# Kernel tuning notes

Hardware: AMD Instinct MI355X
Metric: run time of the kernel (lower is better)

Reference implementation:

```python
import jax, jax.numpy as jnp
import numpy as np

B, S, D, H, DFF = 2, 2048, 2048, 16, 8192
DH = D // H
EPS = 1e-5


def _layer_norm(x, g, b):
    mu = jnp.mean(x, axis=-1, keepdims=True)
    var = jnp.mean(jnp.square(x - mu), axis=-1, keepdims=True)
    return (x - mu) * jax.lax.rsqrt(var + EPS) * g + b


def setup_inputs() -> dict:
    key = jax.random.key(0)
    ks = jax.random.split(key, 12)
    sc = 0.02
    inp = {
        "x": jax.random.normal(ks[0], (B, S, D), dtype=jnp.float32),
        # attention projections, stored [in, out] (torch Linear weight transposed)
        "wq": jax.random.normal(ks[1], (D, D), dtype=jnp.float32) * sc,
        "bq": jnp.zeros((D,), jnp.float32),
        "wk": jax.random.normal(ks[2], (D, D), dtype=jnp.float32) * sc,
        "bk": jnp.zeros((D,), jnp.float32),
        "wv": jax.random.normal(ks[3], (D, D), dtype=jnp.float32) * sc,
        "bv": jnp.zeros((D,), jnp.float32),
        "wo": jax.random.normal(ks[4], (D, D), dtype=jnp.float32) * sc,
        "bo": jnp.zeros((D,), jnp.float32),
        "ln1_g": jnp.ones((D,), jnp.float32),
        "ln1_b": jnp.zeros((D,), jnp.float32),
        # feed-forward
        "w1": jax.random.normal(ks[5], (D, DFF), dtype=jnp.float32) * sc,
        "b1": jnp.zeros((DFF,), jnp.float32),
        "w2": jax.random.normal(ks[6], (DFF, D), dtype=jnp.float32) * sc,
        "b2": jnp.zeros((D,), jnp.float32),
        "ln2_g": jnp.ones((D,), jnp.float32),
        "ln2_b": jnp.zeros((D,), jnp.float32),
    }
    return inp


def reference(x, wq, bq, wk, bk, wv, bv, wo, bo, ln1_g, ln1_b,
              w1, b1, w2, b2, ln2_g, ln2_b):
    # ---- MultiHeadAttentionBlock: x + MHA(LN(x)) ----
    h = _layer_norm(x, ln1_g, ln1_b)                      # [B,S,D]
    q = (h @ wq + bq).reshape(B, S, H, DH).transpose(0, 2, 1, 3)  # [B,H,S,DH]
    k = (h @ wk + bk).reshape(B, S, H, DH).transpose(0, 2, 1, 3)
    v = (h @ wv + bv).reshape(B, S, H, DH).transpose(0, 2, 1, 3)

    # faithful to source: scale by sqrt(d_dim), NOT sqrt(head_dim)
    scores = jnp.einsum("bhqd,bhkd->bhqk", q, k) / np.sqrt(D).astype(np.float32)
    # faithful triu/transpose masking (softmax sees raw zeros, not -inf)
    t = jnp.triu(scores).swapaxes(-2, -1)                 # [B,H,S,S]
    s = jax.nn.softmax(t, axis=-2)
    r = jnp.triu(s).swapaxes(-2, -1)
    attn = jnp.einsum("bhqk,bhkd->bhqd", r, v)            # [B,H,S,DH]
    attn = attn.transpose(0, 2, 1, 3).reshape(B, S, D)
    x = x + attn @ wo + bo

    # ---- FeedForwardBlock: x + FF(LN(x)), dropout rate 0 ----
    h2 = _layer_norm(x, ln2_g, ln2_b)
    ff = jax.nn.relu(h2 @ w1 + b1) @ w2 + b2
    return x + ff
```

## Files before the change

kernel.cpp:

```cpp
#include <hip/hip_runtime.h>


typedef unsigned short ushort_t;
typedef unsigned int   uint32;
typedef __attribute__((ext_vector_type(8)))  short    short8;
typedef __attribute__((ext_vector_type(8)))  ushort_t ushort8;
typedef __attribute__((ext_vector_type(4)))  float    f32x4;

#define BDIM   2
#define SEQ    2048
#define DMODEL 2048
#define NHEAD  16
#define DHEAD  128
#define DFFN   8192
#define MROWS  (BDIM*SEQ)
#define LDQKV  6144

#define GPTR(p) (const __attribute__((address_space(1))) void*)((const void*)(p))
#define SPTR(p) (__attribute__((address_space(3))) void*)((void*)(p))

__device__ __forceinline__ float bf2f(ushort_t u) {
  union { uint32 i; float f; } c; c.i = ((uint32)u) << 16; return c.f;
}
__device__ __forceinline__ ushort_t f2bf(float f) {
  union { float f; uint32 i; } c; c.f = f;
  uint32 u = c.i;
  return (ushort_t)((u + 0x7fffu + ((u >> 16) & 1u)) >> 16);
}

__global__ __launch_bounds__(256) void prep_kern(
    const float* __restrict__ wq, const float* __restrict__ wk,
    const float* __restrict__ wv, const float* __restrict__ wo,
    const float* __restrict__ w1, const float* __restrict__ w2,
    const float* __restrict__ bq, const float* __restrict__ bk,
    const float* __restrict__ bv,
    ushort_t* __restrict__ WQKV, ushort_t* __restrict__ WOT,
    ushort_t* __restrict__ W1T, ushort_t* __restrict__ W2T,
    float* __restrict__ Bcat)
{
  const int bid = blockIdx.x;
  if (bid >= 49152) {
    for (int i = threadIdx.x; i < 6144; i += 256)
      Bcat[i] = (i < 2048) ? bq[i] : ((i < 4096) ? bk[i - 2048] : bv[i - 4096]);
    return;
  }
  const float* W; ushort_t* Wt; int K, N, local;
  if (bid < 12288) {
    const int which = bid >> 12; local = bid & 4095;
    W = (which == 0) ? wq : (which == 1) ? wk : wv;
    Wt = WQKV + (size_t)which * 2048 * 2048; K = 2048; N = 2048;
  } else if (bid < 16384) { W = wo; Wt = WOT; K = 2048; N = 2048; local = bid - 12288; }
  else if (bid < 32768)   { W = w1; Wt = W1T; K = 2048; N = 8192; local = bid - 16384; }
  else                    { W = w2; Wt = W2T; K = 8192; N = 2048; local = bid - 32768; }
  const int ntiles = N >> 5;
  const int nb = (local % ntiles) * 32, kb = (local / ntiles) * 32;

  __shared__ float tile[32][33];
  const int tx = threadIdx.x & 31, ty = threadIdx.x >> 5;
#pragma unroll
  for (int j = 0; j < 32; j += 8)
    tile[ty + j][tx] = W[(size_t)(kb + ty + j) * N + nb + tx];
  __syncthreads();
#pragma unroll
  for (int j = 0; j < 32; j += 8)
    Wt[(size_t)(nb + ty + j) * K + kb + tx] = f2bf(tile[tx][ty + j]);
}

__global__ __launch_bounds__(256) void ln_kern(
    const float* __restrict__ X, const float* __restrict__ G,
    const float* __restrict__ Bb, ushort_t* __restrict__ Out)
{
  const int row = blockIdx.x, tid = threadIdx.x;
  const float* xr = X + (size_t)row * DMODEL;
  float4 v0 = ((const float4*)xr)[tid * 2];
  float4 v1 = ((const float4*)xr)[tid * 2 + 1];
  float s  = v0.x + v0.y + v0.z + v0.w + v1.x + v1.y + v1.z + v1.w;
  float ss = v0.x*v0.x + v0.y*v0.y + v0.z*v0.z + v0.w*v0.w
           + v1.x*v1.x + v1.y*v1.y + v1.z*v1.z + v1.w*v1.w;
#pragma unroll
  for (int off = 32; off > 0; off >>= 1) {
    s  += __shfl_down(s, off);
    ss += __shfl_down(ss, off);
  }
  __shared__ float rs[4], rss[4];
  __shared__ float sh_mu, sh_rst;
  const int wv = tid >> 6;
  if ((tid & 63) == 0) { rs[wv] = s; rss[wv] = ss; }
  __syncthreads();
  if (tid == 0) {
    float S1 = rs[0] + rs[1] + rs[2] + rs[3];
    float S2 = rss[0] + rss[1] + rss[2] + rss[3];
    float mu = S1 * (1.f / DMODEL);
    float var = S2 * (1.f / DMODEL) - mu * mu;
    sh_mu = mu;
    sh_rst = rsqrtf(var + 1e-5f);
  }
  __syncthreads();
  const float mu = sh_mu, rst = sh_rst;
  float4 g0 = ((const float4*)G)[tid * 2];
  float4 g1 = ((const float4*)G)[tid * 2 + 1];
  float4 b0 = ((const float4*)Bb)[tid * 2];
  float4 b1 = ((const float4*)Bb)[tid * 2 + 1];
  ushort8 o;
  o[0] = f2bf((v0.x - mu) * rst * g0.x + b0.x);
  o[1] = f2bf((v0.y - mu) * rst * g0.y + b0.y);
  o[2] = f2bf((v0.z - mu) * rst * g0.z + b0.z);
  o[3] = f2bf((v0.w - mu) * rst * g0.w + b0.w);
  o[4] = f2bf((v1.x - mu) * rst * g1.x + b1.x);
  o[5] = f2bf((v1.y - mu) * rst * g1.y + b1.y);
  o[6] = f2bf((v1.z - mu) * rst * g1.z + b1.z);
  o[7] = f2bf((v1.w - mu) * rst * g1.w + b1.w);
  *(ushort8*)(Out + (size_t)row * DMODEL + tid * 8) = o;
}

__global__ __launch_bounds__(256) void combine_ln_kern(
    const ushort_t* __restrict__ pp, const float* __restrict__ bias,
    const float* __restrict__ xres, const float* __restrict__ G,
    const float* __restrict__ Bb, float* __restrict__ X2,
    ushort_t* __restrict__ Out)
{
  const int row = blockIdx.x, tid = threadIdx.x;
  const size_t i = (size_t)row * DMODEL + tid * 8;
  ushort8 p0 = *(const ushort8*)(pp + i);
  ushort8 p1 = *(const ushort8*)(pp + (size_t)MROWS * 2048 + i);
  float v[8];
#pragma unroll
  for (int j = 0; j < 8; ++j)
    v[j] = bf2f(p0[j]) + bf2f(p1[j]) + bias[tid * 8 + j] + xres[i + j];
  float4 o0 = {v[0], v[1], v[2], v[3]}, o1 = {v[4], v[5], v[6], v[7]};
  *(float4*)(X2 + i) = o0;
  *(float4*)(X2 + i + 4) = o1;

  float s = 0.f, ss = 0.f;
#pragma unroll
  for (int j = 0; j < 8; ++j) { s += v[j]; ss += v[j] * v[j]; }
#pragma unroll
  for (int off = 32; off > 0; off >>= 1) {
    s  += __shfl_down(s, off);
    ss += __shfl_down(ss, off);
  }
  __shared__ float rs[4], rss[4];
  __shared__ float sh_mu, sh_rst;
  const int wvv = tid >> 6;
  if ((tid & 63) == 0) { rs[wvv] = s; rss[wvv] = ss; }
  __syncthreads();
  if (tid == 0) {
    float S1 = rs[0] + rs[1] + rs[2] + rs[3];
    float S2 = rss[0] + rss[1] + rss[2] + rss[3];
    float mu = S1 * (1.f / DMODEL);
    float var = S2 * (1.f / DMODEL) - mu * mu;
    sh_mu = mu; sh_rst = rsqrtf(var + 1e-5f);
  }
  __syncthreads();
  const float mu = sh_mu, rst = sh_rst;
  ushort8 o;
#pragma unroll
  for (int j = 0; j < 8; ++j)
    o[j] = f2bf((v[j] - mu) * rst * G[tid * 8 + j] + Bb[tid * 8 + j]);
  *(ushort8*)(Out + i) = o;
}

template<int OUT, int RELU, int KDIV>
__global__ __launch_bounds__(512, 2) void gemm8_kern(
    const ushort_t* __restrict__ A, const ushort_t* __restrict__ Bt,
    const float* __restrict__ bias, void* __restrict__ Cout,
    int M, int N, int K)
{
  __shared__ ushort_t sA[4 * 8192];
  __shared__ ushort_t sB[4 * 8192];

  const int tid = threadIdx.x;
  const int nM  = gridDim.y;
  const int nwg = gridDim.x * nM;
  const int bid = blockIdx.y * gridDim.x + blockIdx.x;
  const int cpx = nwg >> 3;
  const int swz = (bid & 7) * cpx + (bid >> 3);
  const int m0 = (swz % nM) * 256;
  const int n0 = (swz / nM) * 256;

  const int Keff = K / KDIV;
  const int k0 = (KDIV > 1) ? blockIdx.z * Keff : 0;
  const int T = Keff >> 6;

  const int l = tid & 63, w = tid >> 6;
  const int lr = l & 15, lg = l >> 4;
  const int wr = w >> 2, wc = w & 3;

  const int xch   = (lg ^ ((lr >> 1) & 3)) * 8;
  const int abase = (wr * 128 + lr) * 32 + xch;
  const int bbase = (wc * 64  + lr) * 32 + xch;

  const int sr = tid >> 2;
  const int sg = ((tid & 3) ^ ((tid >> 3) & 3)) * 8;
  const ushort_t* Asrc = A  + (size_t)(m0 + sr) * K + k0 + sg;
  const ushort_t* Bsrc = Bt + (size_t)(n0 + sr) * K + k0 + sg;
  ushort_t* dA = sA + tid * 8;
  ushort_t* dB = sB + tid * 8;

#define SA_(slot, kt, kk, r) __builtin_amdgcn_global_load_lds( \
    GPTR(Asrc + (size_t)(r) * 128 * K + (kt) * 64 + (kk) * 32), \
    SPTR(dA + (slot) * 8192 + (r) * 4096), 16, 0, 0)
#define SB_(slot, kt, kk, r) __builtin_amdgcn_global_load_lds( \
    GPTR(Bsrc + (size_t)(r) * 128 * K + (kt) * 64 + (kk) * 32), \
    SPTR(dB + (slot) * 8192 + (r) * 4096), 16, 0, 0)

  f32x4 acc[8][4] = {};

  SA_(0, 0, 0, 0); SA_(0, 0, 0, 1); SB_(0, 0, 0, 0); SB_(0, 0, 0, 1);
  SA_(1, 0, 1, 0); SA_(1, 0, 1, 1); SB_(1, 0, 1, 0); SB_(1, 0, 1, 1);
  SA_(2, 1, 0, 0); SA_(2, 1, 0, 1); SB_(2, 1, 0, 0); SB_(2, 1, 0, 1);
  asm volatile("s_waitcnt vmcnt(8)" ::: "memory");
  __builtin_amdgcn_s_barrier();

  for (int t = 0; t < T; ++t) {
    const int c = t & 1;
    const ushort_t* A0 = sA + (c * 2 + 0) * 8192;
    const ushort_t* B0 = sB + (c * 2 + 0) * 8192;
    const ushort_t* A1 = sA + (c * 2 + 1) * 8192;
    const ushort_t* B1 = sB + (c * 2 + 1) * 8192;
    const int s1 = (c ^ 1) * 2 + 1;
    const int s0 = c * 2;
    const bool pf1 = (t + 1 < T), pf0 = (t + 2 < T);
    const bool last2 = (t >= T - 2);

    short8 a0, a1, a2, a3, b0, b1, b2, b3;

    b0 = *(const short8*)(B0 + bbase);
    b1 = *(const short8*)(B0 + bbase + 512);
    b2 = *(const short8*)(B0 + bbase + 1024);
    b3 = *(const short8*)(B0 + bbase + 1536);
    a0 = *(const short8*)(A0 + abase);
    a1 = *(const short8*)(A0 + abase + 512);
    a2 = *(const short8*)(A0 + abase + 1024);
    a3 = *(const short8*)(A0 + abase + 1536);
    if (pf1) { SA_(s1, t + 1, 1, 0); SA_(s1, t + 1, 1, 1); }
    __builtin_amdgcn_s_setprio(1);
    acc[0][0] = __builtin_amdgcn_mfma_f32_16x16x32_bf16(a0, b0, acc[0][0], 0, 0, 0);
    acc[0][1] = __builtin_amdgcn_mfma_f32_16x16x32_bf16(a0, b1, acc[0][1], 0, 0, 0);
    acc[0][2] = __builtin_amdgcn_mfma_f32_16x16x32_bf16(a0, b2, acc[0][2], 0, 0, 0);
    acc[0][3] = __builtin_amdgcn_mfma_f32_16x16x32_bf16(a0, b3, acc[0][3], 0, 0, 0);
    acc[1][0] = __builtin_amdgcn_mfma_f32_16x16x32_bf16(a1, b0, acc[1][0], 0, 0, 0);
    acc[1][1] = __builtin_amdgcn_mfma_f32_16x16x32_bf16(a1, b1, acc[1][1], 0, 0, 0);
    acc[1][2] = __builtin_amdgcn_mfma_f32_16x16x32_bf16(a1, b2, acc[1][2], 0, 0, 0);
    acc[1][3] = __builtin_amdgcn_mfma_f32_16x16x32_bf16(a1, b3, acc[1][3], 0, 0, 0);
    acc[2][0] = __builtin_amdgcn_mfma_f32_16x16x32_bf16(a2, b0, acc[2][0], 0, 0, 0);
    acc[2][1] = __builtin_amdgcn_mfma_f32_16x16x32_bf16(a2, b1, acc[2][1], 0, 0, 0);
    acc[2][2] = __builtin_amdgcn_mfma_f32_16x16x32_bf16(a2, b2, acc[2][2], 0, 0, 0);
    acc[2][3] = __builtin_amdgcn_mfma_f32_16x16x32_bf16(a2, b3, acc[2][3], 0, 0, 0);
    acc[3][0] = __builtin_amdgcn_mfma_f32_16x16x32_bf16(a3, b0, acc[3][0], 0, 0, 0);
    acc[3][1] = __builtin_amdgcn_mfma_f32_16x16x32_bf16(a3, b1, acc[3][1], 0, 0, 0);
    acc[3][2] = __builtin_amdgcn_mfma_f32_16x16x32_bf16(a3, b2, acc[3][2], 0, 0, 0);
    acc[3][3] = __builtin_amdgcn_mfma_f32_16x16x32_bf16(a3, b3, acc[3][3], 0, 0, 0);
    __builtin_amdgcn_s_setprio(0);

    a0 = *(const short8*)(A0 + abase + 2048);
    a1 = *(const short8*)(A0 + abase + 2560);
    a2 = *(const short8*)(A0 + abase + 3072);
    a3 = *(const short8*)(A0 + abase + 3584);
    if (pf1) { SB_(s1, t + 1, 1, 0); SB_(s1, t + 1, 1, 1); }
    __builtin_amdgcn_s_setprio(1);
    acc[4][0] = __builtin_amdgcn_mfma_f32_16x16x32_bf16(a0, b0, acc[4][0], 0, 0, 0);
    acc[4][1] = __builtin_amdgcn_mfma_f32_16x16x32_bf16(a0, b1, acc[4][1], 0, 0, 0);
    acc[4][2] = __builtin_amdgcn_mfma_f32_16x16x32_bf16(a0, b2, acc[4][2], 0, 0, 0);
    acc[4][3] = __builtin_amdgcn_mfma_f32_16x16x32_bf16(a0, b3, acc[4][3], 0, 0, 0);
    acc[5][0] = __builtin_amdgcn_mfma_f32_16x16x32_bf16(a1, b0, acc[5][0], 0, 0, 0);
    acc[5][1] = __builtin_amdgcn_mfma_f32_16x16x32_bf16(a1, b1, acc[5][1], 0, 0, 0);
    acc[5][2] = __builtin_amdgcn_mfma_f32_16x16x32_bf16(a1, b2, acc[5][2], 0, 0, 0);
    acc[5][3] = __builtin_amdgcn_mfma_f32_16x16x32_bf16(a1, b3, acc[5][3], 0, 0, 0);
    acc[6][0] = __builtin_amdgcn_mfma_f32_16x16x32_bf16(a2, b0, acc[6][0], 0, 0, 0);
    acc[6][1] = __builtin_amdgcn_mfma_f32_16x16x32_bf16(a2, b1, acc[6][1], 0, 0, 0);
    acc[6][2] = __builtin_amdgcn_mfma_f32_16x16x32_bf16(a2, b2, acc[6][2], 0, 0, 0);
    acc[6][3] = __builtin_amdgcn_mfma_f32_16x16x32_bf16(a2, b3, acc[6][3], 0, 0, 0);
    acc[7][0] = __builtin_amdgcn_mfma_f32_16x16x32_bf16(a3, b0, acc[7][0], 0, 0, 0);
    acc[7][1] = __builtin_amdgcn_mfma_f32_16x16x32_bf16(a3, b1, acc[7][1], 0, 0, 0);
    acc[7][2] = __builtin_amdgcn_mfma_f32_16x16x32_bf16(a3, b2, acc[7][2], 0, 0, 0);
    acc[7][3] = __builtin_amdgcn_mfma_f32_16x16x32_bf16(a3, b3, acc[7][3], 0, 0, 0);
    __builtin_amdgcn_s_setprio(0);
    if (!last2) { asm volatile("s_waitcnt vmcnt(8)" ::: "memory"); }
    else        { asm volatile("s_waitcnt vmcnt(0)" ::: "memory"); }
    __builtin_amdgcn_s_barrier();

    b0 = *(const short8*)(B1 + bbase);
    b1 = *(const short8*)(B1 + bbase + 512);
    b2 = *(const short8*)(B1 + bbase + 1024);
    b3 = *(const short8*)(B1 + bbase + 1536);
    a0 = *(const short8*)(A1 + abase);
    a1 = *(const short8*)(A1 + abase + 512);
    a2 = *(const short8*)(A1 + abase + 1024);
    a3 = *(const short8*)(A1 + abase + 1536);
    if (pf0) { SA_(s0, t + 2, 0, 0); SA_(s0, t + 2, 0, 1); }
    __builtin_amdgcn_s_setprio(1);
    acc[0][0] = __builtin_amdgcn_mfma_f32_16x16x32_bf16(a0, b0, acc[0][0], 0, 0, 0);
    acc[0][1] = __builtin_amdgcn_mfma_f32_16x16x32_bf16(a0, b1, acc[0][1], 0, 0, 0);
    acc[0][2] = __builtin_amdgcn_mfma_f32_16x16x32_bf16(a0, b2, acc[0][2], 0, 0, 0);
    acc[0][3] = __builtin_amdgcn_mfma_f32_16x16x32_bf16(a0, b3, acc[0][3], 0, 0, 0);
    acc[1][0] = __builtin_amdgcn_mfma_f32_16x16x32_bf16(a1, b0, acc[1][0], 0, 0, 0);
    acc[1][1] = __builtin_amdgcn_mfma_f32_16x16x32_bf16(a1, b1, acc[1][1], 0, 0, 0);
    acc[1][2] = __builtin_amdgcn_mfma_f32_16x16x32_bf16(a1, b2, acc[1][2], 0, 0, 0);
    acc[1][3] = __builtin_amdgcn_mfma_f32_16x16x32_bf16(a1, b3, acc[1][3], 0, 0, 0);
    acc[2][0] = __builtin_amdgcn_mfma_f32_16x16x32_bf16(a2, b0, acc[2][0], 0, 0, 0);
    acc[2][1] = __builtin_amdgcn_mfma_f32_16x16x32_bf16(a2, b1, acc[2][1], 0, 0, 0);
    acc[2][2] = __builtin_amdgcn_mfma_f32_16x16x32_bf16(a2, b2, acc[2][2], 0, 0, 0);
    acc[2][3] = __builtin_amdgcn_mfma_f32_16x16x32_bf16(a2, b3, acc[2][3], 0, 0, 0);
    acc[3][0] = __builtin_amdgcn_mfma_f32_16x16x32_bf16(a3, b0, acc[3][0], 0, 0, 0);
    acc[3][1] = __builtin_amdgcn_mfma_f32_16x16x32_bf16(a3, b1, acc[3][1], 0, 0, 0);
    acc[3][2] = __builtin_amdgcn_mfma_f32_16x16x32_bf16(a3, b2, acc[3][2], 0, 0, 0);
    acc[3][3] = __builtin_amdgcn_mfma_f32_16x16x32_bf16(a3, b3, acc[3][3], 0, 0, 0);
    __builtin_amdgcn_s_setprio(0);

    a0 = *(const short8*)(A1 + abase + 2048);
    a1 = *(const short8*)(A1 + abase + 2560);
    a2 = *(const short8*)(A1 + abase + 3072);
    a3 = *(const short8*)(A1 + abase + 3584);
    if (pf0) { SB_(s0, t + 2, 0, 0); SB_(s0, t + 2, 0, 1); }
    __builtin_amdgcn_s_setprio(1);
    acc[4][0] = __builtin_amdgcn_mfma_f32_16x16x32_bf16(a0, b0, acc[4][0], 0, 0, 0);
    acc[4][1] = __builtin_amdgcn_mfma_f32_16x16x32_bf16(a0, b1, acc[4][1], 0, 0, 0);
    acc[4][2] = __builtin_amdgcn_mfma_f32_16x16x32_bf16(a0, b2, acc[4][2], 0, 0, 0);
    acc[4][3] = __builtin_amdgcn_mfma_f32_16x16x32_bf16(a0, b3, acc[4][3], 0, 0, 0);
    acc[5][0] = __builtin_amdgcn_mfma_f32_16x16x32_bf16(a1, b0, acc[5][0], 0, 0, 0);
    acc[5][1] = __builtin_amdgcn_mfma_f32_16x16x32_bf16(a1, b1, acc[5][1], 0, 0, 0);
    acc[5][2] = __builtin_amdgcn_mfma_f32_16x16x32_bf16(a1, b2, acc[5][2], 0, 0, 0);
    acc[5][3] = __builtin_amdgcn_mfma_f32_16x16x32_bf16(a1, b3, acc[5][3], 0, 0, 0);
    acc[6][0] = __builtin_amdgcn_mfma_f32_16x16x32_bf16(a2, b0, acc[6][0], 0, 0, 0);
    acc[6][1] = __builtin_amdgcn_mfma_f32_16x16x32_bf16(a2, b1, acc[6][1], 0, 0, 0);
    acc[6][2] = __builtin_amdgcn_mfma_f32_16x16x32_bf16(a2, b2, acc[6][2], 0, 0, 0);
    acc[6][3] = __builtin_amdgcn_mfma_f32_16x16x32_bf16(a2, b3, acc[6][3], 0, 0, 0);
    acc[7][0] = __builtin_amdgcn_mfma_f32_16x16x32_bf16(a3, b0, acc[7][0], 0, 0, 0);
    acc[7][1] = __builtin_amdgcn_mfma_f32_16x16x32_bf16(a3, b1, acc[7][1], 0, 0, 0);
    acc[7][2] = __builtin_amdgcn_mfma_f32_16x16x32_bf16(a3, b2, acc[7][2], 0, 0, 0);
    acc[7][3] = __builtin_amdgcn_mfma_f32_16x16x32_bf16(a3, b3, acc[7][3], 0, 0, 0);
    __builtin_amdgcn_s_setprio(0);
    if (!last2) { asm volatile("s_waitcnt vmcnt(8)" ::: "memory"); }
    else        { asm volatile("s_waitcnt vmcnt(0)" ::: "memory"); }
    __builtin_amdgcn_s_barrier();
  }
#undef SA_
#undef SB_

  ushort_t* Pz = (OUT == 2)
      ? (ushort_t*)Cout + (size_t)blockIdx.z * M * N : (ushort_t*)Cout;
#pragma unroll
  for (int mi = 0; mi < 8; ++mi) {
#pragma unroll
    for (int ni = 0; ni < 4; ++ni) {
      const int gn = n0 + wc * 64 + ni * 16 + lr;
      const float bvv = (OUT == 2) ? 0.f : bias[gn];
#pragma unroll
      for (int j = 0; j < 4; ++j) {
        const int gm = m0 + wr * 128 + mi * 16 + lg * 4 + j;
        float v = acc[mi][ni][j] + bvv;
        if (RELU) v = fmaxf(v, 0.f);
        Pz[(size_t)gm * N + gn] = f2bf(v);
      }
    }
  }
}

template<int RELU>
__global__ __launch_bounds__(512) void gemm_hi_kern(
    const ushort_t* __restrict__ A, const ushort_t* __restrict__ Bt,
    const float* __restrict__ bias, ushort_t* __restrict__ Cout,
    int M, int N, int K)
{
  __shared__ ushort_t sA[3 * 4096];
  __shared__ ushort_t sB[3 * 8192];

  const int tid = threadIdx.x;
  const int nM  = gridDim.y;
  const int nwg = gridDim.x * nM;
  const int bid = blockIdx.y * gridDim.x + blockIdx.x;
  const int cpx = nwg >> 3;
  const int swz = (bid & 7) * cpx + (bid >> 3);
  const int m0 = (swz % nM) * 128;
  const int n0 = (swz / nM) * 256;

  const int l = tid & 63, w = tid >> 6;
  const int lr = l & 15, lg = l >> 4;
  const int wr = w >> 2, wc = w & 3;

  const int xch   = (lg ^ ((lr >> 1) & 3)) * 8;
  const int abase = (wr * 64 + lr) * 32 + xch;
  const int bbase = (wc * 64 + lr) * 32 + xch;

  const int sr = tid >> 2;
  const int sg = ((tid & 3) ^ ((tid >> 3) & 3)) * 8;
  const ushort_t* Asrc = A  + (size_t)(m0 + sr) * K + sg;
  const ushort_t* Bsrc = Bt + (size_t)(n0 + sr) * K + sg;
  ushort_t* dA = sA + tid * 8;
  ushort_t* dB = sB + tid * 8;

  const int U = K >> 5;

#define SAU(slot, u) __builtin_amdgcn_global_load_lds( \
    GPTR(Asrc + (size_t)(u) * 32), SPTR(dA + (slot) * 4096), 16, 0, 0)
#define SBU(slot, u, r) __builtin_amdgcn_global_load_lds( \
    GPTR(Bsrc + (size_t)(r) * 128 * K + (size_t)(u) * 32), \
    SPTR(dB + (slot) * 8192 + (r) * 4096), 16, 0, 0)

  f32x4 acc[4][4] = {};

  SAU(0, 0); SBU(0, 0, 0); SBU(0, 0, 1);
  SAU(1, 1); SBU(1, 1, 0); SBU(1, 1, 1);
  asm volatile("s_waitcnt vmcnt(3)" ::: "memory");
  __builtin_amdgcn_s_barrier();

  int cur = 0;
  for (int u = 0; u < U; ++u) {
    const ushort_t* pA = sA + cur * 4096;
    const ushort_t* pB = sB + cur * 8192;
    const int nx = (cur == 0) ? 2 : cur - 1;
    short8 af[4], bf[4];
#pragma unroll
    for (int i = 0; i < 4; ++i) af[i] = *(const short8*)(pA + abase + i * 512);
#pragma unroll
    for (int i = 0; i < 4; ++i) bf[i] = *(const short8*)(pB + bbase + i * 512);
    if (u + 2 < U) { SAU(nx, u + 2); SBU(nx, u + 2, 0); SBU(nx, u + 2, 1); }
    __builtin_amdgcn_s_setprio(1);
#pragma unroll
    for (int mi = 0; mi < 4; ++mi)
#pragma unroll
      for (int ni = 0; ni < 4; ++ni)
        acc[mi][ni] = __builtin_amdgcn_mfma_f32_16x16x32_bf16(
            af[mi], bf[ni], acc[mi][ni], 0, 0, 0);
    __builtin_amdgcn_s_setprio(0);
    if (u < U - 2) { asm volatile("s_waitcnt vmcnt(3)" ::: "memory"); }
    else           { asm volatile("s_waitcnt vmcnt(0)" ::: "memory"); }
    __builtin_amdgcn_s_barrier();
    cur = (cur == 2) ? 0 : cur + 1;
  }
#undef SAU
#undef SBU

#pragma unroll
  for (int mi = 0; mi < 4; ++mi) {
#pragma unroll
    for (int ni = 0; ni < 4; ++ni) {
      const int gn = n0 + wc * 64 + ni * 16 + lr;
      const float bvv = bias[gn];
#pragma unroll
      for (int j = 0; j < 4; ++j) {
        const int gm = m0 + wr * 64 + mi * 16 + lg * 4 + j;
        float v = acc[mi][ni][j] + bvv;
        if (RELU) v = fmaxf(v, 0.f);
        Cout[(size_t)gm * N + gn] = f2bf(v);
      }
    }
  }
}

__global__ __launch_bounds__(256) void combine_kern(
    const ushort_t* __restrict__ pp, const float* __restrict__ bias,
    const float* __restrict__ resid, float* __restrict__ out)
{
  const size_t i = ((size_t)blockIdx.x * 256 + threadIdx.x) * 8;
  ushort8 p0 = *(const ushort8*)(pp + i);
  ushort8 p1 = *(const ushort8*)(pp + (size_t)MROWS * 2048 + i);
  const int col = (int)(i & 2047);
  float4 r0 = *(const float4*)(resid + i);
  float4 r1 = *(const float4*)(resid + i + 4);
  float4 c0 = *(const float4*)(bias + col);
  float4 c1 = *(const float4*)(bias + col + 4);
  float4 o0, o1;
  o0.x = bf2f(p0[0]) + bf2f(p1[0]) + c0.x + r0.x;
  o0.y = bf2f(p0[1]) + bf2f(p1[1]) + c0.y + r0.y;
  o0.z = bf2f(p0[2]) + bf2f(p1[2]) + c0.z + r0.z;
  o0.w = bf2f(p0[3]) + bf2f(p1[3]) + c0.w + r0.w;
  o1.x = bf2f(p0[4]) + bf2f(p1[4]) + c1.x + r1.x;
  o1.y = bf2f(p0[5]) + bf2f(p1[5]) + c1.y + r1.y;
  o1.z = bf2f(p0[6]) + bf2f(p1[6]) + c1.z + r1.z;
  o1.w = bf2f(p0[7]) + bf2f(p1[7]) + c1.w + r1.w;
  *(float4*)(out + i) = o0;
  *(float4*)(out + i + 4) = o1;
}

__global__ __launch_bounds__(256) void attn_stats_kern(
    const ushort_t* __restrict__ Q, const ushort_t* __restrict__ Kb,
    float* __restrict__ E, float* __restrict__ DG, int ld)
{
  __shared__ ushort_t Ksm[64 * 128];
  const int qb = blockIdx.x;
  const int bh = blockIdx.y;
  const int b = bh >> 4, h = bh & 15;
  const int tid = threadIdx.x;
  const int l = tid & 63, w = tid >> 6;
  const int lr = l & 15, lg = l >> 4;

  const int qrow0 = qb * 128 + w * 32;

  short8 af[2][4];
#pragma unroll
  for (int g = 0; g < 2; ++g) {
    const size_t qoff = (size_t)(b * SEQ + qrow0 + g * 16 + lr) * ld + h * DHEAD + lg * 8;
#pragma unroll
    for (int c = 0; c < 4; ++c) af[g][c] = *(const short8*)(Q + qoff + c * 32);
  }

  const int srow_b = w * 16 + (l >> 4);
  const ushort_t* Kg = Kb + (size_t)b * SEQ * ld + (size_t)h * DHEAD;
  ushort_t* Sbase = Ksm + w * 2048;

  f32x4 sume[2] = {{0.f,0.f,0.f,0.f},{0.f,0.f,0.f,0.f}};
  f32x4 dge[2]  = {{0.f,0.f,0.f,0.f},{0.f,0.f,0.f,0.f}};
  const float scale = 0.0220970869120796f;
  const int rx = lr & 7;

  for (int kc = qb * 2; kc < 32; ++kc) {
    __syncthreads();
#pragma unroll
    for (int c = 0; c < 4; ++c) {
      const int row = srow_b + c * 4;
      const int g = (l & 15) ^ (row & 7);
      __builtin_amdgcn_global_load_lds(
          GPTR(Kg + (size_t)(kc * 64 + row) * ld + g * 8),
          SPTR(Sbase + c * 512), 16, 0, 0);
    }
    __syncthreads();

    for (int ks = 0; ks < 4; ++ks) {
      const int kbase = kc * 64 + ks * 16;
      if (kbase + 16 <= qrow0) continue;
      short8 bfr[4];
#pragma unroll
      for (int c = 0; c < 4; ++c)
        bfr[c] = *(const short8*)(Ksm + (ks * 16 + lr) * 128 + ((lg + c * 4) ^ rx) * 8);
#pragma unroll
      for (int g = 0; g < 2; ++g) {
        const int qg = qrow0 + g * 16;
        if (kbase < qg) continue;
        f32x4 sc = {0.f, 0.f, 0.f, 0.f};
        sc = __builtin_amdgcn_mfma_f32_16x16x32_bf16(af[g][0], bfr[0], sc, 0, 0, 0);
        sc = __builtin_amdgcn_mfma_f32_16x16x32_bf16(af[g][1], bfr[1], sc, 0, 0, 0);
        sc = __builtin_amdgcn_mfma_f32_16x16x32_bf16(af[g][2], bfr[2], sc, 0, 0, 0);
        sc = __builtin_amdgcn_mfma_f32_16x16x32_bf16(af[g][3], bfr[3], sc, 0, 0, 0);
        if (kbase == qg) {
          const int ki = kbase + lr;
#pragma unroll
          for (int j = 0; j < 4; ++j) {
            const int qi = qg + lg * 4 + j;
            if (ki >= qi) {
              float e = __expf(sc[j] * scale);
              sume[g][j] += e;
              if (ki == qi) dge[g][j] += e;
            }
          }
        } else {
#pragma unroll
          for (int j = 0; j < 4; ++j)
            sume[g][j] += __expf(sc[j] * scale);
        }
      }
    }
  }

#pragma unroll
  for (int g = 0; g < 2; ++g) {
#pragma unroll
    for (int j = 0; j < 4; ++j) {
#pragma unroll
      for (int off = 1; off < 16; off <<= 1) {
        sume[g][j] += __shfl_xor(sume[g][j], off);
        dge[g][j]  += __shfl_xor(dge[g][j], off);
      }
    }
  }
  if (lr == 0) {
#pragma unroll
    for (int g = 0; g < 2; ++g)
#pragma unroll
      for (int j = 0; j < 4; ++j) {
        E[(size_t)bh * SEQ + qrow0 + g * 16 + lg * 4 + j]  = sume[g][j];
        DG[(size_t)bh * SEQ + qrow0 + g * 16 + lg * 4 + j] = dge[g][j];
      }
  }
}

__global__ __launch_bounds__(128) void vchunk_kern(
    const ushort_t* __restrict__ V, float* __restrict__ CS, int ld)
{
  const int c = blockIdx.x, bh = blockIdx.y;
  const int b = bh >> 4, h = bh & 15;
  const int dh = threadIdx.x;
  const ushort_t* vp = V + (size_t)(b * SEQ + c * 64) * ld + h * DHEAD + dh;
  float s = 0.f;
  for (int i = 0; i < 64; ++i) s += bf2f(vp[(size_t)i * ld]);
  CS[((size_t)bh * 32 + c) * 128 + dh] = s;
}

__global__ __launch_bounds__(128) void attn_combine_kern(
    const ushort_t* __restrict__ V, const float* __restrict__ CS,
    const float* __restrict__ E, const float* __restrict__ DG,
    ushort_t* __restrict__ Attn, int ldv)
{
  const int c = blockIdx.x, bh = blockIdx.y;
  const int b = bh >> 4, h = bh & 15;
  const int dh = threadIdx.x;
  float prefix = 0.f;
  for (int cc = 0; cc < c; ++cc) prefix += CS[((size_t)bh * 32 + cc) * 128 + dh];
  const ushort_t* vp = V + (size_t)(b * SEQ + c * 64) * ldv + h * DHEAD + dh;
  ushort_t* ap = Attn + (size_t)(b * SEQ + c * 64) * DMODEL + h * DHEAD + dh;
  const int qb = c * 64;
  for (int i = 0; i < 64; ++i) {
    const int qq = qb + i;
    const float denom = (float)qq + E[(size_t)bh * SEQ + qq];
    const float de = DG[(size_t)bh * SEQ + qq];
    const float vv = bf2f(vp[(size_t)i * ldv]);
    ap[(size_t)i * DMODEL] = f2bf((prefix + de * vv) / denom);
    prefix += vv;
  }
}

extern "C" void kernel_launch(void* const* d_in, const int* in_sizes, int n_in,
                              void* d_out, int out_size, void* d_ws, size_t ws_size,
                              hipStream_t stream)
{
  const float* x    = (const float*)d_in[0];
  const float* wq   = (const float*)d_in[1];
  const float* bq   = (const float*)d_in[2];
  const float* wk   = (const float*)d_in[3];
  const float* bk   = (const float*)d_in[4];
  const float* wv   = (const float*)d_in[5];
  const float* bv   = (const float*)d_in[6];
  const float* wo   = (const float*)d_in[7];
  const float* bo   = (const float*)d_in[8];
  const float* ln1g = (const float*)d_in[9];
  const float* ln1b = (const float*)d_in[10];
  const float* w1   = (const float*)d_in[11];
  const float* b1   = (const float*)d_in[12];
  const float* w2   = (const float*)d_in[13];
  const float* b2   = (const float*)d_in[14];
  const float* ln2g = (const float*)d_in[15];
  const float* ln2b = (const float*)d_in[16];
  float* out = (float*)d_out;

  char* ws = (char*)d_ws;
  ushort_t* W1T  = (ushort_t*)(ws + 0);
  ushort_t* PPf2 = (ushort_t*)(ws + 0);
  ushort_t* W2T  = (ushort_t*)(ws + 33554432);
  ushort_t* WOT  = (ushort_t*)(ws + 67108864);
  float*    X2   = (float*)   (ws + 75497472);
  float*    Bcat = (float*)   (ws + 75497472);
  ushort_t* Hb   = (ushort_t*)(ws + 109051904);
  ushort_t* F1   = (ushort_t*)(ws + 125829120);
  ushort_t* PPwo = (ushort_t*)(ws + 125829120);
  ushort_t* WQKV = (ushort_t*)(ws + 125829120);
  ushort_t* QKVb = (ushort_t*)(ws + 150994944);
  float*    Eb   = (float*)   (ws + 201326592);
  float*    DGb  = (float*)   (ws + 201588736);
  float*    CSb  = (float*)   (ws + 201850880);

  prep_kern<<<49153, 256, 0, stream>>>(wq, wk, wv, wo, w1, w2, bq, bk, bv,
                                       WQKV, WOT, W1T, W2T, Bcat);

  ln_kern<<<MROWS, 256, 0, stream>>>(x, ln1g, ln1b, Hb);

  gemm8_kern<1, 0, 1><<<dim3(24, 16), 512, 0, stream>>>(
      Hb, WQKV, Bcat, QKVb, MROWS, LDQKV, DMODEL);

  attn_stats_kern<<<dim3(16, 32), 256, 0, stream>>>(QKVb, QKVb + 2048, Eb, DGb, LDQKV);

  vchunk_kern<<<dim3(32, 32), 128, 0, stream>>>(QKVb + 4096, CSb, LDQKV);
  attn_combine_kern<<<dim3(32, 32), 128, 0, stream>>>(QKVb + 4096, CSb, Eb, DGb, Hb, LDQKV);

  gemm8_kern<2, 0, 2><<<dim3(8, 16, 2), 512, 0, stream>>>(
      Hb, WOT, bo, PPwo, MROWS, DMODEL, DMODEL);

  combine_ln_kern<<<MROWS, 256, 0, stream>>>(PPwo, bo, x, ln2g, ln2b, X2, Hb);

  gemm_hi_kern<1><<<dim3(32, 32), 512, 0, stream>>>(
      Hb, W1T, b1, F1, MROWS, DFFN, DMODEL);

  gemm8_kern<2, 0, 2><<<dim3(8, 16, 2), 512, 0, stream>>>(
      F1, W2T, b2, PPf2, MROWS, DMODEL, DFFN);
  combine_kern<<<4096, 256, 0, stream>>>(PPf2, b2, X2, out);
}
```

Measured before the change: 631.4 us.

## Swap GEMM tile configs per layer and double-buffer K tiles in attention stats

The QKV and output-projection GEMMs now use the 128x256 three-stage kernel, which gains split-K support. The FFN1 GEMM moves to the 256x256 kernel. The attention stats kernel now double-buffers K tiles in shared memory, so the next chunk's load overlaps the current chunk's MFMA work. A residual/fp32-output path is added to gemm8 but is not used. These changes rebalance grid sizes and occupancy per GEMM shape and hide load latency in the attention pass, at the cost of more shared memory in attn_stats.

```diff
diff --git a/kernel.cpp b/kernel.cpp
--- a/kernel.cpp
+++ b/kernel.cpp
@@ -160,11 +160,11 @@
   *(ushort8*)(Out + i) = o;
 }
 
-template<int OUT, int RELU, int KDIV>
+template<int OUT, int RELU, int RESID, int KDIV>
 __global__ __launch_bounds__(512, 2) void gemm8_kern(
     const ushort_t* __restrict__ A, const ushort_t* __restrict__ Bt,
-    const float* __restrict__ bias, void* __restrict__ Cout,
-    int M, int N, int K)
+    const float* __restrict__ bias, const float* __restrict__ resid,
+    void* __restrict__ Cout, int M, int N, int K)
 {
   __shared__ ushort_t sA[4 * 8192];
   __shared__ ushort_t sB[4 * 8192];
@@ -350,14 +350,16 @@
       for (int j = 0; j < 4; ++j) {
         const int gm = m0 + wr * 128 + mi * 16 + lg * 4 + j;
         float v = acc[mi][ni][j] + bvv;
+        if (RESID) v += resid[(size_t)gm * N + gn];
         if (RELU) v = fmaxf(v, 0.f);
-        Pz[(size_t)gm * N + gn] = f2bf(v);
+        if (OUT == 0)      ((float*)Cout)[(size_t)gm * N + gn] = v;
+        else               Pz[(size_t)gm * N + gn] = f2bf(v);
       }
     }
   }
 }
 
-template<int RELU>
+template<int OUT, int RELU, int KDIV>
 __global__ __launch_bounds__(512) void gemm_hi_kern(
     const ushort_t* __restrict__ A, const ushort_t* __restrict__ Bt,
     const float* __restrict__ bias, ushort_t* __restrict__ Cout,
@@ -375,6 +377,10 @@
   const int m0 = (swz % nM) * 128;
   const int n0 = (swz / nM) * 256;
 
+  const int Keff = K / KDIV;
+  const int k0 = (KDIV > 1) ? blockIdx.z * Keff : 0;
+  const int U = Keff >> 5;
+
   const int l = tid & 63, w = tid >> 6;
   const int lr = l & 15, lg = l >> 4;
   const int wr = w >> 2, wc = w & 3;
@@ -385,12 +391,10 @@
 
   const int sr = tid >> 2;
   const int sg = ((tid & 3) ^ ((tid >> 3) & 3)) * 8;
-  const ushort_t* Asrc = A  + (size_t)(m0 + sr) * K + sg;
-  const ushort_t* Bsrc = Bt + (size_t)(n0 + sr) * K + sg;
+  const ushort_t* Asrc = A  + (size_t)(m0 + sr) * K + k0 + sg;
+  const ushort_t* Bsrc = Bt + (size_t)(n0 + sr) * K + k0 + sg;
   ushort_t* dA = sA + tid * 8;
   ushort_t* dB = sB + tid * 8;
-
-  const int U = K >> 5;
 
 #define SAU(slot, u) __builtin_amdgcn_global_load_lds( \
     GPTR(Asrc + (size_t)(u) * 32), SPTR(dA + (slot) * 4096), 16, 0, 0)
@@ -432,18 +436,20 @@
 #undef SAU
 #undef SBU
 
+  ushort_t* Pz = (OUT == 2)
+      ? Cout + (size_t)blockIdx.z * M * N : Cout;
 #pragma unroll
   for (int mi = 0; mi < 4; ++mi) {
 #pragma unroll
     for (int ni = 0; ni < 4; ++ni) {
       const int gn = n0 + wc * 64 + ni * 16 + lr;
-      const float bvv = bias[gn];
+      const float bvv = (OUT == 2) ? 0.f : bias[gn];
 #pragma unroll
       for (int j = 0; j < 4; ++j) {
         const int gm = m0 + wr * 64 + mi * 16 + lg * 4 + j;
         float v = acc[mi][ni][j] + bvv;
         if (RELU) v = fmaxf(v, 0.f);
-        Cout[(size_t)gm * N + gn] = f2bf(v);
+        Pz[(size_t)gm * N + gn] = f2bf(v);
       }
     }
   }
@@ -478,7 +484,7 @@
     const ushort_t* __restrict__ Q, const ushort_t* __restrict__ Kb,
     float* __restrict__ E, float* __restrict__ DG, int ld)
 {
-  __shared__ ushort_t Ksm[64 * 128];
+  __shared__ ushort_t Ksm[2 * 8192];
   const int qb = blockIdx.x;
   const int bh = blockIdx.y;
   const int b = bh >> 4, h = bh & 15;
@@ -498,24 +504,30 @@
 
   const int srow_b = w * 16 + (l >> 4);
   const ushort_t* Kg = Kb + (size_t)b * SEQ * ld + (size_t)h * DHEAD;
-  ushort_t* Sbase = Ksm + w * 2048;
 
   f32x4 sume[2] = {{0.f,0.f,0.f,0.f},{0.f,0.f,0.f,0.f}};
   f32x4 dge[2]  = {{0.f,0.f,0.f,0.f},{0.f,0.f,0.f,0.f}};
   const float scale = 0.0220970869120796f;
   const int rx = lr & 7;
-
-  for (int kc = qb * 2; kc < 32; ++kc) {
-    __syncthreads();
-#pragma unroll
-    for (int c = 0; c < 4; ++c) {
-      const int row = srow_b + c * 4;
-      const int g = (l & 15) ^ (row & 7);
-      __builtin_amdgcn_global_load_lds(
-          GPTR(Kg + (size_t)(kc * 64 + row) * ld + g * 8),
-          SPTR(Sbase + c * 512), 16, 0, 0);
-    }
-    __syncthreads();
+  const int kc0 = qb * 2;
+
+#define STAGEK(kc, buf) do { \
+    _Pragma("unroll") \
+    for (int c_ = 0; c_ < 4; ++c_) { \
+      const int row_ = srow_b + c_ * 4; \
+      const int g_ = (l & 15) ^ (row_ & 7); \
+      __builtin_amdgcn_global_load_lds( \
+          GPTR(Kg + (size_t)((kc) * 64 + row_) * ld + g_ * 8), \
+          SPTR(Ksm + (buf) * 8192 + w * 2048 + c_ * 512), 16, 0, 0); \
+    } } while (0)
+
+  STAGEK(kc0, 0);
+  __syncthreads();
+
+  int cur = 0;
+  for (int kc = kc0; kc < 32; ++kc) {
+    if (kc + 1 < 32) STAGEK(kc + 1, cur ^ 1);
+    const ushort_t* Kbuf = Ksm + cur * 8192;
 
     for (int ks = 0; ks < 4; ++ks) {
       const int kbase = kc * 64 + ks * 16;
@@ -523,7 +535,7 @@
       short8 bfr[4];
 #pragma unroll
       for (int c = 0; c < 4; ++c)
-        bfr[c] = *(const short8*)(Ksm + (ks * 16 + lr) * 128 + ((lg + c * 4) ^ rx) * 8);
+        bfr[c] = *(const short8*)(Kbuf + (ks * 16 + lr) * 128 + ((lg + c * 4) ^ rx) * 8);
 #pragma unroll
       for (int g = 0; g < 2; ++g) {
         const int qg = qrow0 + g * 16;
@@ -551,7 +563,10 @@
         }
       }
     }
-  }
+    __syncthreads();
+    cur ^= 1;
+  }
+#undef STAGEK
 
 #pragma unroll
   for (int g = 0; g < 2; ++g) {
@@ -654,7 +669,7 @@
 
   ln_kern<<<MROWS, 256, 0, stream>>>(x, ln1g, ln1b, Hb);
 
-  gemm8_kern<1, 0, 1><<<dim3(24, 16), 512, 0, stream>>>(
+  gemm_hi_kern<1, 0, 1><<<dim3(24, 32), 512, 0, stream>>>(
       Hb, WQKV, Bcat, QKVb, MROWS, LDQKV, DMODEL);
 
   attn_stats_kern<<<dim3(16, 32), 256, 0, stream>>>(QKVb, QKVb + 2048, Eb, DGb, LDQKV);
@@ -662,15 +677,15 @@
   vchunk_kern<<<dim3(32, 32), 128, 0, stream>>>(QKVb + 4096, CSb, LDQKV);
   attn_combine_kern<<<dim3(32, 32), 128, 0, stream>>>(QKVb + 4096, CSb, Eb, DGb, Hb, LDQKV);
 
-  gemm8_kern<2, 0, 2><<<dim3(8, 16, 2), 512, 0, stream>>>(
+  gemm_hi_kern<2, 0, 2><<<dim3(8, 32, 2), 512, 0, stream>>>(
       Hb, WOT, bo, PPwo, MROWS, DMODEL, DMODEL);
 
   combine_ln_kern<<<MROWS, 256, 0, stream>>>(PPwo, bo, x, ln2g, ln2b, X2, Hb);
 
-  gemm_hi_kern<1><<<dim3(32, 32), 512, 0, stream>>>(
-      Hb, W1T, b1, F1, MROWS, DFFN, DMODEL);
-
-  gemm8_kern<2, 0, 2><<<dim3(8, 16, 2), 512, 0, stream>>>(
-      F1, W2T, b2, PPf2, MROWS, DMODEL, DFFN);
+  gemm8_kern<1, 1, 0, 1><<<dim3(32, 16), 512, 0, stream>>>(
+      Hb, W1T, b1, nullptr, F1, MROWS, DFFN, DMODEL);
+
+  gemm8_kern<2, 0, 0, 2><<<dim3(8, 16, 2), 512, 0, stream>>>(
+      F1, W2T, b2, nullptr, PPf2, MROWS, DMODEL, DFFN);
   combine_kern<<<4096, 256, 0, stream>>>(PPf2, b2, X2, out);
 }
```

Result: faster. 603.6 us (median of 2 runs) (-4.4%).
